# Performance work log

Hardware: AMD Instinct MI355X
Metric: run time of the kernel (lower is better)

Reference implementation:

```python
import jax, jax.numpy as jnp
import numpy as np

N_HEAD = 16
D_MODEL = 1024
D_K = 64
D_V = 64
EPS = 1e-5  # nn.LayerNorm default


def setup_inputs() -> dict:
    key = jax.random.key(0)
    ks = jax.random.split(key, 12)
    B, L, T = 2, 2048, 2048
    std_qk = np.sqrt(2.0 / (D_MODEL + D_K)).astype(np.float32)
    std_v = np.sqrt(2.0 / (D_MODEL + D_V)).astype(np.float32)
    # xavier_normal for fc: std = sqrt(2 / (fan_in + fan_out))
    std_fc = np.sqrt(2.0 / (N_HEAD * D_V + D_MODEL)).astype(np.float32)
    return {
        "q": jax.random.normal(ks[0], (B, L, D_MODEL), jnp.float32),
        "k": jax.random.normal(ks[1], (B, T, D_MODEL), jnp.float32),
        "v": jax.random.normal(ks[2], (B, T, D_MODEL), jnp.float32),
        # torch Linear weight is (out, in); apply as x @ W.T
        "w_q": jax.random.normal(ks[3], (N_HEAD * D_K, D_MODEL), jnp.float32) * std_qk,
        "b_q": jnp.zeros((N_HEAD * D_K,), jnp.float32),
        "w_k": jax.random.normal(ks[4], (N_HEAD * D_K, D_MODEL), jnp.float32) * std_qk,
        "b_k": jnp.zeros((N_HEAD * D_K,), jnp.float32),
        "w_v": jax.random.normal(ks[5], (N_HEAD * D_V, D_MODEL), jnp.float32) * std_v,
        "b_v": jnp.zeros((N_HEAD * D_V,), jnp.float32),
        "w_fc": jax.random.normal(ks[6], (D_MODEL, N_HEAD * D_V), jnp.float32) * std_fc,
        "b_fc": jnp.zeros((D_MODEL,), jnp.float32),
        "gamma": jnp.ones((D_MODEL,), jnp.float32),
        "beta": jnp.zeros((D_MODEL,), jnp.float32),
    }


def reference(q, k, v, w_q, b_q, w_k, b_k, w_v, b_v, w_fc, b_fc, gamma, beta):
    B, L, _ = q.shape
    T = k.shape[1]
    residual = q
    qh = (q @ w_q.T + b_q).reshape(B, L, N_HEAD, D_K)  # b l h k
    kh = (k @ w_k.T + b_k).reshape(B, T, N_HEAD, D_K)  # b t h k
    vh = (v @ w_v.T + b_v).reshape(B, T, N_HEAD, D_V)  # b t h v
    attn = jnp.einsum('blhk,bthk->blht', qh, kh) / jnp.sqrt(jnp.asarray(D_K, qh.dtype))
    attn = jax.nn.softmax(attn, axis=3)
    out = jnp.einsum('blht,bthv->blhv', attn, vh).reshape(B, L, N_HEAD * D_V)
    out = out @ w_fc.T + b_fc  # dropout is identity in eval mode
    x = out + residual
    mu = jnp.mean(x, axis=-1, keepdims=True)
    var = jnp.var(x, axis=-1, keepdims=True)
    out = (x - mu) / jnp.sqrt(var + EPS) * gamma + beta
    return out, attn
```

## Files before the change

### kernel.cpp

```cpp
#include <hip/hip_runtime.h>
#include <stdint.h>
#include <stddef.h>


typedef __attribute__((ext_vector_type(8))) short short8;
typedef __attribute__((ext_vector_type(4))) short short4v;
typedef __attribute__((ext_vector_type(4))) float f32x4;

#define MFMA16 __builtin_amdgcn_mfma_f32_16x16x32_bf16

__device__ __forceinline__ float bf2f(short s) {
    union { unsigned u; float f; } c; c.u = ((unsigned)(unsigned short)s) << 16; return c.f;
}
__device__ __forceinline__ unsigned short f2bf(float x) {
    union { float f; unsigned u; } c; c.f = x;
    unsigned r = (c.u + 0x7FFFu + ((c.u >> 16) & 1u)) >> 16;
    return (unsigned short)r;
}
__device__ __forceinline__ unsigned pk2(float a, float b) {
    return (unsigned)f2bf(a) | ((unsigned)f2bf(b) << 16);
}
__device__ __forceinline__ short8 ld8f(const float* p) {
    const f32x4 x = *(const f32x4*)p, y = *(const f32x4*)(p + 4);
    short8 r;
    r[0] = (short)f2bf(x[0]); r[1] = (short)f2bf(x[1]);
    r[2] = (short)f2bf(x[2]); r[3] = (short)f2bf(x[3]);
    r[4] = (short)f2bf(y[0]); r[5] = (short)f2bf(y[1]);
    r[6] = (short)f2bf(y[2]); r[7] = (short)f2bf(y[3]);
    return r;
}
__device__ __forceinline__ void gll16(const short* g, short* l) {
    __builtin_amdgcn_global_load_lds(
        (const __attribute__((address_space(1))) unsigned int*)g,
        (__attribute__((address_space(3))) unsigned int*)l,
        16, 0, 0);
}

__global__ __launch_bounds__(256)
void cvt_k(const float* __restrict__ s0, const float* __restrict__ s1,
           const float* __restrict__ s2, const float* __restrict__ s3,
           const float* __restrict__ s4, const float* __restrict__ s5,
           const float* __restrict__ s6,
           short* __restrict__ d0, short* __restrict__ d1, short* __restrict__ d2,
           short* __restrict__ d3, short* __restrict__ d4, short* __restrict__ d5,
           short* __restrict__ d6)
{
    const int t = blockIdx.y;
    const float* s; short* d; int n;
    switch (t) {
        case 0: s = s0; d = d0; n = 4194304; break;
        case 1: s = s1; d = d1; n = 4194304; break;
        case 2: s = s2; d = d2; n = 4194304; break;
        case 3: s = s3; d = d3; n = 1048576; break;
        case 4: s = s4; d = d4; n = 1048576; break;
        case 5: s = s5; d = d5; n = 1048576; break;
        default: s = s6; d = d6; n = 1048576; break;
    }
    const int idx = (blockIdx.x * 256 + threadIdx.x) * 8;
    if (idx < n) *(short8*)(d + idx) = ld8f(s + idx);
}

template<int OP>
__global__ __launch_bounds__(256)
void gemm_k(const short* __restrict__ A0, const short* __restrict__ A1, const short* __restrict__ A2,
            const short* __restrict__ W0, const short* __restrict__ W1, const short* __restrict__ W2,
            const float* __restrict__ bz0, const float* __restrict__ bz1, const float* __restrict__ bz2,
            short* __restrict__ D0, short* __restrict__ D1, short* __restrict__ D2,
            const float* __restrict__ resid, short* __restrict__ yout)
{
    __shared__ short lds[2][8192];
    const int tid = threadIdx.x;
    const int lane = tid & 63, w = tid >> 6;
    const int rl = lane & 15, q = lane >> 4;
    const int m0 = blockIdx.x * 128, n0 = blockIdx.y * 128;
    const int wrow = (w >> 1) * 64, wcol = (w & 1) * 64;

    const short *Ag, *Wg; const float* bias; short* dst; int zm;
    if (OP == 0) {
        const int z = blockIdx.z;
        Ag  = (z == 0) ? A0 : (z == 1) ? A1 : A2;
        Wg  = (z == 0) ? W0 : (z == 1) ? W1 : W2;
        bias= (z == 0) ? bz0 : (z == 1) ? bz1 : bz2;
        dst = (z == 0) ? D0 : (z == 1) ? D1 : D2;
        zm  = (z == 2) ? 1 : 0;
    } else {
        Ag = A0; Wg = W0; bias = bz0; dst = yout; zm = 2;
    }

    f32x4 acc[4][4];
    #pragma unroll
    for (int a = 0; a < 4; ++a)
      #pragma unroll
      for (int b = 0; b < 4; ++b) acc[a][b] = (f32x4){0.f, 0.f, 0.f, 0.f};

    const int sr0 = (w * 2 + 0) * 16 + (lane >> 2);
    const int sr1 = (w * 2 + 1) * 16 + (lane >> 2);
    const int sc  = (lane & 3) * 8;

    #define STAGE(buf, kt)                                                        \
        gll16(Ag + (size_t)(m0 + sr0) * 1024 + (kt) + sc, &lds[buf][(w*2+0)*512]);\
        gll16(Ag + (size_t)(m0 + sr1) * 1024 + (kt) + sc, &lds[buf][(w*2+1)*512]);\
        gll16(Wg + (size_t)(n0 + sr0) * 1024 + (kt) + sc, &lds[buf][4096+(w*2+0)*512]);\
        gll16(Wg + (size_t)(n0 + sr1) * 1024 + (kt) + sc, &lds[buf][4096+(w*2+1)*512]);

    STAGE(0, 0);
    __syncthreads();
    int cur = 0;
    for (int kt = 0; kt < 1024; kt += 32) {
        if (kt + 32 < 1024) { STAGE(cur ^ 1, kt + 32); }
        short8 af[4], bfv[4];
        #pragma unroll
        for (int mt = 0; mt < 4; ++mt)
            af[mt] = *(const short8*)&lds[cur][(wrow + mt * 16 + rl) * 32 + q * 8];
        #pragma unroll
        for (int nt = 0; nt < 4; ++nt)
            bfv[nt] = *(const short8*)&lds[cur][4096 + (wcol + nt * 16 + rl) * 32 + q * 8];
        #pragma unroll
        for (int mt = 0; mt < 4; ++mt)
          #pragma unroll
          for (int nt = 0; nt < 4; ++nt)
            acc[mt][nt] = MFMA16(af[mt], bfv[nt], acc[mt][nt], 0, 0, 0);
        __syncthreads();
        cur ^= 1;
    }
    #undef STAGE

    float biasv[4];
    #pragma unroll
    for (int nt = 0; nt < 4; ++nt) biasv[nt] = bias[n0 + wcol + nt * 16 + rl];

    short* ldsF = &lds[0][0];

    if (zm == 0) {
        #pragma unroll
        for (int pass = 0; pass < 2; ++pass) {
            if ((w >> 1) == pass) {
                #pragma unroll
                for (int mt = 0; mt < 4; ++mt)
                  #pragma unroll
                  for (int nt = 0; nt < 4; ++nt) {
                    const int col = wcol + nt * 16 + rl;
                    #pragma unroll
                    for (int i = 0; i < 4; ++i)
                        ldsF[(mt * 16 + q * 4 + i) * 136 + col] =
                            (short)f2bf(acc[mt][nt][i] + biasv[nt]);
                  }
            }
            __syncthreads();
            {
                const int hrun = tid >> 7, idx = tid & 127;
                const int lr = idx >> 1, ch = idx & 1;
                const int gm = m0 + pass * 64 + lr;
                const int bb = gm >> 11, ll = gm & 2047;
                const int h = (n0 + hrun * 64) >> 6;
                short* dstp = dst + (((size_t)(bb * 16 + h) * 2048) + ll) * 64 + ch * 32;
                const short* srcp = &ldsF[lr * 136 + hrun * 64 + ch * 32];
                #pragma unroll
                for (int c = 0; c < 4; ++c)
                    *(short8*)(dstp + c * 8) = *(const short8*)(srcp + c * 8);
            }
            __syncthreads();
        }
    } else if (zm == 1) {
        const int bb = m0 >> 11, t0 = m0 & 2047;
        #pragma unroll
        for (int pass = 0; pass < 2; ++pass) {
            if ((w & 1) == pass) {
                #pragma unroll
                for (int nt = 0; nt < 4; ++nt) {
                    const int lcol = nt * 16 + rl;
                    #pragma unroll
                    for (int mt = 0; mt < 4; ++mt) {
                        const int mloc = wrow + mt * 16 + q * 4;
                        const unsigned lo = pk2(acc[mt][nt][0] + biasv[nt],
                                                acc[mt][nt][1] + biasv[nt]);
                        const unsigned hi = pk2(acc[mt][nt][2] + biasv[nt],
                                                acc[mt][nt][3] + biasv[nt]);
                        *(unsigned long long*)&ldsF[lcol * 136 + mloc] =
                            (unsigned long long)lo | ((unsigned long long)hi << 32);
                    }
                }
            }
            __syncthreads();
            {
                const int lcol = tid >> 2, mch = tid & 3;
                const int gn = n0 + pass * 64 + lcol;
                const int h = gn >> 6, dv = gn & 63;
                short* dstp = dst + ((size_t)(bb * 16 + h) * 64 + dv) * 2048 + t0 + mch * 32;
                const short* srcp = &ldsF[lcol * 136 + mch * 32];
                #pragma unroll
                for (int c = 0; c < 4; ++c)
                    *(short8*)(dstp + c * 8) = *(const short8*)(srcp + c * 8);
            }
            __syncthreads();
        }
    } else {
        #pragma unroll
        for (int pass = 0; pass < 2; ++pass) {
            if ((w >> 1) == pass) {
                #pragma unroll
                for (int mt = 0; mt < 4; ++mt)
                  #pragma unroll
                  for (int nt = 0; nt < 4; ++nt) {
                    const int col = wcol + nt * 16 + rl;
                    #pragma unroll
                    for (int i = 0; i < 4; ++i)
                        ldsF[(mt * 16 + q * 4 + i) * 136 + col] =
                            (short)f2bf(acc[mt][nt][i] + biasv[nt]);
                  }
            }
            __syncthreads();
            {
                const int lr = tid >> 2, ch = tid & 3;
                const int gm = m0 + pass * 64 + lr;
                const float* rp = resid + (size_t)gm * 1024 + n0 + ch * 32;
                short* dstp = dst + (size_t)gm * 1024 + n0 + ch * 32;
                const short* srcp = &ldsF[lr * 136 + ch * 32];
                #pragma unroll
                for (int c = 0; c < 4; ++c) {
                    const short8 v = *(const short8*)(srcp + c * 8);
                    const f32x4 r0 = *(const f32x4*)(rp + c * 8);
                    const f32x4 r1 = *(const f32x4*)(rp + c * 8 + 4);
                    short8 o;
                    #pragma unroll
                    for (int j = 0; j < 4; ++j) {
                        o[j]     = (short)f2bf(bf2f(v[j])     + r0[j]);
                        o[4 + j] = (short)f2bf(bf2f(v[4 + j]) + r1[j]);
                    }
                    *(short8*)(dstp + c * 8) = o;
                }
            }
            __syncthreads();
        }
    }
}

__device__ __forceinline__ void attn_swz(int j, int& rb, int& bh) {
    const int xcd = j & 7, k2 = j >> 3;
    rb = k2 & 15;
    bh = (xcd << 2) | (k2 >> 4);
}

__global__ __launch_bounds__(512)
void attn_fused(const short* __restrict__ qh, const short* __restrict__ kh,
                const short* __restrict__ vhT,
                float* __restrict__ attn, short* __restrict__ Obf)
{
    __shared__ short ldsK[128 * 72];
    __shared__ short ldsV[64 * 136];
    __shared__ short ldsP[8][16 * 72];
    const int tid = threadIdx.x, lane = tid & 63, w = tid >> 6;
    const int rl = lane & 15, q = lane >> 4;
    int rb, bh; attn_swz(blockIdx.x, rb, bh);
    const int r = rb * 128 + w * 16 + rl;
    const int b = bh >> 4, h = bh & 15;

    const size_t qoff = ((size_t)bh * 2048 + r) * 64;
    const short8 bq0 = *(const short8*)(qh + qoff + q * 8);
    const short8 bq1 = *(const short8*)(qh + qoff + 32 + q * 8);

    const size_t kbase = (size_t)bh * 2048 * 64;
    const size_t vbase = (size_t)bh * 64 * 2048;
    const int srow = tid >> 2, soff = (tid & 3) * 16;
    const int vrow = tid >> 3, voff = (tid & 7) * 16;
    const size_t abaseW = (((size_t)b * 2048 + rb * 128 + w * 16) * 16 + h) * 2048;

    float ls0 = 0.f, ls1 = 0.f, ls2 = 0.f, ls3 = 0.f;
    short8 kst[2], vst[2];
    {
        const short* src = kh + kbase + (size_t)srow * 64 + soff;
        kst[0] = *(const short8*)src;
        kst[1] = *(const short8*)(src + 8);
    }
    for (int it = 0; it < 16; ++it) {
        __syncthreads();
        *(short8*)&ldsK[srow * 72 + soff]     = kst[0];
        *(short8*)&ldsK[srow * 72 + soff + 8] = kst[1];
        __syncthreads();
        if (it < 15) {
            const short* src = kh + kbase + (size_t)(((it + 1) << 7) + srow) * 64 + soff;
            kst[0] = *(const short8*)src;
            kst[1] = *(const short8*)(src + 8);
        }
        #pragma unroll
        for (int tt = 0; tt < 8; ++tt) {
            const short* kr = &ldsK[(tt * 16 + rl) * 72];
            const short8 ak0 = *(const short8*)(kr + q * 8);
            const short8 ak1 = *(const short8*)(kr + 32 + q * 8);
            f32x4 st = MFMA16(ak0, bq0, (f32x4){0.f, 0.f, 0.f, 0.f}, 0, 0, 0);
            st = MFMA16(ak1, bq1, st, 0, 0, 0);
            ls0 += __expf(st[0] * 0.125f - 12.f);
            ls1 += __expf(st[1] * 0.125f - 12.f);
            ls2 += __expf(st[2] * 0.125f - 12.f);
            ls3 += __expf(st[3] * 0.125f - 12.f);
        }
    }
    float ls = (ls0 + ls1) + (ls2 + ls3);
    ls += __shfl_xor(ls, 16);
    ls += __shfl_xor(ls, 32);
    const float linv = 1.f / ls;

    f32x4 acc[4];
    #pragma unroll
    for (int dt = 0; dt < 4; ++dt) acc[dt] = (f32x4){0.f, 0.f, 0.f, 0.f};

    {
        const short* ks = kh + kbase + (size_t)srow * 64 + soff;
        const short* vs = vhT + vbase + (size_t)vrow * 2048 + voff;
        kst[0] = *(const short8*)ks;  kst[1] = *(const short8*)(ks + 8);
        vst[0] = *(const short8*)vs;  vst[1] = *(const short8*)(vs + 8);
    }
    for (int it = 0; it < 16; ++it) {
        const int t0 = it << 7;
        __syncthreads();
        *(short8*)&ldsK[srow * 72 + soff]      = kst[0];
        *(short8*)&ldsK[srow * 72 + soff + 8]  = kst[1];
        *(short8*)&ldsV[vrow * 136 + voff]     = vst[0];
        *(short8*)&ldsV[vrow * 136 + voff + 8] = vst[1];
        __syncthreads();
        if (it < 15) {
            const short* ks = kh + kbase + (size_t)(t0 + 128 + srow) * 64 + soff;
            const short* vs = vhT + vbase + (size_t)vrow * 2048 + t0 + 128 + voff;
            kst[0] = *(const short8*)ks;  kst[1] = *(const short8*)(ks + 8);
            vst[0] = *(const short8*)vs;  vst[1] = *(const short8*)(vs + 8);
        }
        #pragma unroll
        for (int hh = 0; hh < 4; ++hh) {
            float pv[8];
            #pragma unroll
            for (int sub = 0; sub < 2; ++sub) {
                const int tt = hh * 2 + sub;
                const short* kr = &ldsK[(tt * 16 + rl) * 72];
                const short8 ak0 = *(const short8*)(kr + q * 8);
                const short8 ak1 = *(const short8*)(kr + 32 + q * 8);
                f32x4 st = MFMA16(ak0, bq0, (f32x4){0.f, 0.f, 0.f, 0.f}, 0, 0, 0);
                st = MFMA16(ak1, bq1, st, 0, 0, 0);
                #pragma unroll
                for (int i = 0; i < 4; ++i)
                    pv[sub * 4 + i] = __expf(st[i] * 0.125f - 12.f) * linv;
            }
            short8 pb;
            #pragma unroll
            for (int j = 0; j < 8; ++j) pb[j] = (short)f2bf(pv[j]);
            {
                const int lc = (hh & 1) * 32;
                short4v plo, phi;
                plo[0] = pb[0]; plo[1] = pb[1]; plo[2] = pb[2]; plo[3] = pb[3];
                phi[0] = pb[4]; phi[1] = pb[5]; phi[2] = pb[6]; phi[3] = pb[7];
                *(short4v*)&ldsP[w][rl * 72 + lc + q * 4] = plo;
                *(short4v*)&ldsP[w][rl * 72 + lc + 16 + q * 4] = phi;
            }
            #pragma unroll
            for (int dt = 0; dt < 4; ++dt) {
                const short* vr = &ldsV[(dt * 16 + rl) * 136 + hh * 32];
                const short4v vlo = *(const short4v*)(vr + q * 4);
                const short4v vhi = *(const short4v*)(vr + 16 + q * 4);
                short8 va;
                va[0] = vlo[0]; va[1] = vlo[1]; va[2] = vlo[2]; va[3] = vlo[3];
                va[4] = vhi[0]; va[5] = vhi[1]; va[6] = vhi[2]; va[7] = vhi[3];
                acc[dt] = MFMA16(va, pb, acc[dt], 0, 0, 0);
            }
            if ((hh & 1) && attn != nullptr) {
                const int hcol = hh >> 1;
                const int c8 = (lane & 7) * 8;
                #pragma unroll
                for (int pass = 0; pass < 2; ++pass) {
                    const int rloc = pass * 8 + (lane >> 3);
                    const short8 p8 = *(const short8*)&ldsP[w][rloc * 72 + c8];
                    float* dstp = attn + abaseW + (size_t)rloc * 32768 + t0 + hcol * 64 + c8;
                    f32x4 o0, o1;
                    #pragma unroll
                    for (int j = 0; j < 4; ++j) {
                        o0[j] = bf2f(p8[j]);
                        o1[j] = bf2f(p8[4 + j]);
                    }
                    *(f32x4*)dstp = o0;
                    *(f32x4*)(dstp + 4) = o1;
                }
            }
        }
    }

    #pragma unroll
    for (int dt = 0; dt < 4; ++dt) {
        const int dv0 = dt * 16 + q * 4;
        const unsigned lo = pk2(acc[dt][0], acc[dt][1]);
        const unsigned hi = pk2(acc[dt][2], acc[dt][3]);
        const size_t oidx = ((size_t)b * 2048 + r) * 1024 + h * 64 + dv0;
        *(unsigned long long*)&Obf[oidx] =
            (unsigned long long)lo | ((unsigned long long)hi << 32);
    }
}

__global__ __launch_bounds__(256)
void ln_k(const short* __restrict__ ybf, const float* __restrict__ gamma,
          const float* __restrict__ beta, float* __restrict__ out)
{
    const int tid = threadIdx.x, lane = tid & 63, w = tid >> 6;
    const int row = blockIdx.x * 4 + w;
    const short* yr = ybf + (size_t)row * 1024 + lane * 16;
    const short8 v0 = *(const short8*)(yr);
    const short8 v1 = *(const short8*)(yr + 8);
    float x[16];
    #pragma unroll
    for (int j = 0; j < 8; ++j) { x[j] = bf2f(v0[j]); x[8 + j] = bf2f(v1[j]); }
    float s = 0.f, s2 = 0.f;
    #pragma unroll
    for (int j = 0; j < 16; ++j) { s += x[j]; s2 += x[j] * x[j]; }
    #pragma unroll
    for (int off = 1; off < 64; off <<= 1) {
        s  += __shfl_xor(s, off);
        s2 += __shfl_xor(s2, off);
    }
    const float mean = s * (1.f / 1024.f);
    const float var  = s2 * (1.f / 1024.f) - mean * mean;
    const float rs   = rsqrtf(var + 1e-5f);
    float* orow = out + (size_t)row * 1024 + lane * 16;
    #pragma unroll
    for (int j4 = 0; j4 < 4; ++j4) {
        f32x4 o;
        #pragma unroll
        for (int e = 0; e < 4; ++e) {
            const int c = lane * 16 + j4 * 4 + e;
            o[e] = (x[j4 * 4 + e] - mean) * rs * gamma[c] + beta[c];
        }
        *(f32x4*)(orow + j4 * 4) = o;
    }
}

extern "C" void kernel_launch(void* const* d_in, const int* in_sizes, int n_in,
                              void* d_out, int out_size, void* d_ws, size_t ws_size,
                              hipStream_t stream)
{
    (void)in_sizes; (void)n_in;
    const float* qin  = (const float*)d_in[0];
    const float* kin  = (const float*)d_in[1];
    const float* vin  = (const float*)d_in[2];
    const float* wq   = (const float*)d_in[3];
    const float* b_q  = (const float*)d_in[4];
    const float* wk   = (const float*)d_in[5];
    const float* b_k  = (const float*)d_in[6];
    const float* wv   = (const float*)d_in[7];
    const float* b_v  = (const float*)d_in[8];
    const float* wfc  = (const float*)d_in[9];
    const float* b_fc = (const float*)d_in[10];
    const float* gamma= (const float*)d_in[11];
    const float* beta = (const float*)d_in[12];

    float* out0 = (float*)d_out;
    float* attn = (out_size >= 138412032) ? (out0 + (size_t)4194304) : nullptr;

    short* ws   = (short*)d_ws;
    short* qcb  = ws;
    short* kcb  = qcb + 4194304;
    short* vcb  = kcb + 4194304;
    short* wqb  = vcb + 4194304;
    short* wkb  = wqb + 1048576;
    short* wvb  = wkb + 1048576;
    short* wfcb = wvb + 1048576;
    short* qhb  = wfcb + 1048576;
    short* khb  = qhb + 4194304;
    short* vhTb = khb + 4194304;
    short* Obf  = vhTb + 4194304;
    short* ybf  = Obf + 4194304;
    const size_t need = (size_t)(8 * 4194304 + 4 * 1048576) * 2;
    if (ws_size < need) return;

    cvt_k<<<dim3(2048, 7), 256, 0, stream>>>(
        qin, kin, vin, wq, wk, wv, wfc, qcb, kcb, vcb, wqb, wkb, wvb, wfcb);
    gemm_k<0><<<dim3(32, 8, 3), 256, 0, stream>>>(
        qcb, kcb, vcb, wqb, wkb, wvb, b_q, b_k, b_v, qhb, khb, vhTb,
        nullptr, nullptr);
    attn_fused<<<512, 512, 0, stream>>>(qhb, khb, vhTb, attn, Obf);
    gemm_k<1><<<dim3(32, 8, 1), 256, 0, stream>>>(
        Obf, nullptr, nullptr, wfcb, nullptr, nullptr, b_fc, nullptr, nullptr,
        nullptr, nullptr, nullptr, qin, ybf);
    ln_k<<<1024, 256, 0, stream>>>(ybf, gamma, beta, out0);
}
```

Measured before the change: 264.0 us.

## Read K and V directly from global memory instead of staging through LDS

Removes the shared-memory staging of K and V tiles, together with the register prefetch and the two block barriers per iteration, in both attention passes. Each wave now loads its MFMA operands straight from global memory and relies on the L1/L2 caches for reuse across the 8 waves of a block. This cuts LDS traffic, LDS footprint and synchronisation, but every wave issues its own global loads. Those loads are smaller and less coalesced, which may raise memory latency and cache pressure.

```diff
diff --git a/kernel.cpp b/kernel.cpp
--- a/kernel.cpp
+++ b/kernel.cpp
@@ -246,8 +246,6 @@
                 const short* __restrict__ vhT,
                 float* __restrict__ attn, short* __restrict__ Obf)
 {
-    __shared__ short ldsK[128 * 72];
-    __shared__ short ldsV[64 * 136];
     __shared__ short ldsP[8][16 * 72];
     const int tid = threadIdx.x, lane = tid & 63, w = tid >> 6;
     const int rl = lane & 15, q = lane >> 4;
@@ -261,30 +259,13 @@
 
     const size_t kbase = (size_t)bh * 2048 * 64;
     const size_t vbase = (size_t)bh * 64 * 2048;
-    const int srow = tid >> 2, soff = (tid & 3) * 16;
-    const int vrow = tid >> 3, voff = (tid & 7) * 16;
     const size_t abaseW = (((size_t)b * 2048 + rb * 128 + w * 16) * 16 + h) * 2048;
 
     float ls0 = 0.f, ls1 = 0.f, ls2 = 0.f, ls3 = 0.f;
-    short8 kst[2], vst[2];
-    {
-        const short* src = kh + kbase + (size_t)srow * 64 + soff;
-        kst[0] = *(const short8*)src;
-        kst[1] = *(const short8*)(src + 8);
-    }
-    for (int it = 0; it < 16; ++it) {
-        __syncthreads();
-        *(short8*)&ldsK[srow * 72 + soff]     = kst[0];
-        *(short8*)&ldsK[srow * 72 + soff + 8] = kst[1];
-        __syncthreads();
-        if (it < 15) {
-            const short* src = kh + kbase + (size_t)(((it + 1) << 7) + srow) * 64 + soff;
-            kst[0] = *(const short8*)src;
-            kst[1] = *(const short8*)(src + 8);
-        }
+    for (int t0 = 0; t0 < 2048; t0 += 128) {
         #pragma unroll
         for (int tt = 0; tt < 8; ++tt) {
-            const short* kr = &ldsK[(tt * 16 + rl) * 72];
+            const short* kr = kh + kbase + (size_t)(t0 + tt * 16 + rl) * 64;
             const short8 ak0 = *(const short8*)(kr + q * 8);
             const short8 ak1 = *(const short8*)(kr + 32 + q * 8);
             f32x4 st = MFMA16(ak0, bq0, (f32x4){0.f, 0.f, 0.f, 0.f}, 0, 0, 0);
@@ -304,33 +285,15 @@
     #pragma unroll
     for (int dt = 0; dt < 4; ++dt) acc[dt] = (f32x4){0.f, 0.f, 0.f, 0.f};
 
-    {
-        const short* ks = kh + kbase + (size_t)srow * 64 + soff;
-        const short* vs = vhT + vbase + (size_t)vrow * 2048 + voff;
-        kst[0] = *(const short8*)ks;  kst[1] = *(const short8*)(ks + 8);
-        vst[0] = *(const short8*)vs;  vst[1] = *(const short8*)(vs + 8);
-    }
     for (int it = 0; it < 16; ++it) {
         const int t0 = it << 7;
-        __syncthreads();
-        *(short8*)&ldsK[srow * 72 + soff]      = kst[0];
-        *(short8*)&ldsK[srow * 72 + soff + 8]  = kst[1];
-        *(short8*)&ldsV[vrow * 136 + voff]     = vst[0];
-        *(short8*)&ldsV[vrow * 136 + voff + 8] = vst[1];
-        __syncthreads();
-        if (it < 15) {
-            const short* ks = kh + kbase + (size_t)(t0 + 128 + srow) * 64 + soff;
-            const short* vs = vhT + vbase + (size_t)vrow * 2048 + t0 + 128 + voff;
-            kst[0] = *(const short8*)ks;  kst[1] = *(const short8*)(ks + 8);
-            vst[0] = *(const short8*)vs;  vst[1] = *(const short8*)(vs + 8);
-        }
         #pragma unroll
         for (int hh = 0; hh < 4; ++hh) {
             float pv[8];
             #pragma unroll
             for (int sub = 0; sub < 2; ++sub) {
                 const int tt = hh * 2 + sub;
-                const short* kr = &ldsK[(tt * 16 + rl) * 72];
+                const short* kr = kh + kbase + (size_t)(t0 + tt * 16 + rl) * 64;
                 const short8 ak0 = *(const short8*)(kr + q * 8);
                 const short8 ak1 = *(const short8*)(kr + 32 + q * 8);
                 f32x4 st = MFMA16(ak0, bq0, (f32x4){0.f, 0.f, 0.f, 0.f}, 0, 0, 0);
@@ -352,7 +315,7 @@
             }
             #pragma unroll
             for (int dt = 0; dt < 4; ++dt) {
-                const short* vr = &ldsV[(dt * 16 + rl) * 136 + hh * 32];
+                const short* vr = vhT + vbase + (size_t)(dt * 16 + rl) * 2048 + t0 + hh * 32;
                 const short4v vlo = *(const short4v*)(vr + q * 4);
                 const short4v vhi = *(const short4v*)(vr + 16 + q * 4);
                 short8 va;
```

Result: slower. 594.9 us (+125.3%).
